# Optimization experiments

Hardware: AMD Instinct MI355X
Metric: run time of the kernel (lower is better)

The kernel has to match this reference:

```python
import jax, jax.numpy as jnp
import numpy as np

NEG_SLOPE = 0.01  # torch nn.LeakyReLU default

N_NODES = 100000
N_EDGES = 1000000
D_FEAT = 64


def setup_inputs() -> dict:
    key = jax.random.key(0)
    ks = jax.random.split(key, 8)
    x = jax.random.normal(ks[0], (N_NODES, D_FEAT), dtype=jnp.float32)
    src = jax.random.randint(ks[1], (N_EDGES,), 0, N_NODES, dtype=jnp.int64 if jax.config.jax_enable_x64 else jnp.int32)
    dst = jax.random.randint(ks[2], (N_EDGES,), 0, N_NODES, dtype=jnp.int64 if jax.config.jax_enable_x64 else jnp.int32)
    s = 1.0 / np.sqrt(D_FEAT)
    W1 = jax.random.normal(ks[3], (D_FEAT, 64), dtype=jnp.float32) * s
    b1 = jnp.zeros((64,), dtype=jnp.float32)
    W2 = jax.random.normal(ks[4], (64, 64), dtype=jnp.float32) * s
    b2 = jnp.zeros((64,), dtype=jnp.float32)
    Wc = jax.random.normal(ks[5], (64, 2), dtype=jnp.float32) * s
    bc = jnp.zeros((2,), dtype=jnp.float32)
    return {"x": x, "src": src, "dst": dst, "W1": W1, "b1": b1,
            "W2": W2, "b2": b2, "Wc": Wc, "bc": bc}


def _graph_conv(x, src, dst, W, b, out_deg_isqrt, in_deg_isqrt, n_nodes):
    # DGL GraphConv, norm='both': h_v = ( sum_{u->v} x_u / sqrt(d_out(u)) ) / sqrt(d_in(v)) @ W + b
    # (in_feats <= out_feats here, so aggregate first then transform, matching DGL order)
    h = x * out_deg_isqrt[:, None]          # [N, d] scale by source out-degree
    msg = h[src]                            # [E, d] gather
    agg = jax.ops.segment_sum(msg, dst, num_segments=n_nodes)  # [N, d] scatter-add
    agg = agg * in_deg_isqrt[:, None]
    return agg @ W + b


def reference(x, src, dst, W1, b1, W2, b2, Wc, bc):
    n = x.shape[0]
    ones_e = jnp.ones(src.shape[0], dtype=x.dtype)
    out_deg = jnp.clip(jax.ops.segment_sum(ones_e, src, num_segments=n), 1.0)
    in_deg = jnp.clip(jax.ops.segment_sum(ones_e, dst, num_segments=n), 1.0)
    out_isqrt = out_deg ** -0.5
    in_isqrt = in_deg ** -0.5

    h = _graph_conv(x, src, dst, W1, b1, out_isqrt, in_isqrt, n)
    h = jax.nn.leaky_relu(h, NEG_SLOPE)
    h = _graph_conv(h, src, dst, W2, b2, out_isqrt, in_isqrt, n)
    h = jax.nn.leaky_relu(h, NEG_SLOPE)
    return h @ Wc + bc  # prediction=True -> linear classifier
```

## Files before the change

### kernel.cpp

```cpp
#include <hip/hip_runtime.h>


typedef __attribute__((ext_vector_type(8))) short short8;
typedef __attribute__((ext_vector_type(4))) float f32x4;

#define NPB 256
#define BSH 9
#define BW  512

__device__ __forceinline__ float b2f(unsigned short u) {
    return __uint_as_float(((unsigned int)u) << 16);
}
__device__ __forceinline__ unsigned short f2b(float f) {
    unsigned int i = __float_as_uint(f);
    unsigned int r = (i + 0x7FFFu + ((i >> 16) & 1u)) >> 16;
    return (unsigned short)r;
}

__global__ __launch_bounds__(256) void count_kernel(
    const int* __restrict__ src, const int* __restrict__ dst,
    int* __restrict__ cntD, int* __restrict__ cntS, int e, int chunk) {
    __shared__ int hD[256], hS[256];
    int t = threadIdx.x, pb = blockIdx.x;
    hD[t] = 0; hS[t] = 0;
    __syncthreads();
    int e0 = pb * chunk, e1 = min(e, e0 + chunk);
    for (int i = e0 + t; i < e1; i += 256) {
        atomicAdd(&hD[dst[i] >> BSH], 1);
        atomicAdd(&hS[src[i] >> BSH], 1);
    }
    __syncthreads();
    cntD[t * NPB + pb] = hD[t];
    cntS[t * NPB + pb] = hS[t];
}

__global__ __launch_bounds__(1024) void scanmat_kernel(int* __restrict__ cntD,
                                                       int* __restrict__ cntS) {
    int* a = (blockIdx.x == 0) ? cntD : cntS;
    __shared__ int s[1024];
    int t = threadIdx.x;
    int base = t * 64;
    int sum = 0;
    for (int j = 0; j < 64; j++) sum += a[base + j];
    s[t] = sum;
    __syncthreads();
    for (int d = 1; d < 1024; d <<= 1) {
        int x = (t >= d) ? s[t - d] : 0;
        __syncthreads();
        s[t] += x;
        __syncthreads();
    }
    int run = s[t] - sum;
    for (int j = 0; j < 64; j++) {
        int v = a[base + j];
        a[base + j] = run;
        run += v;
    }
}

__global__ __launch_bounds__(256) void part_kernel(
    const int* __restrict__ src, const int* __restrict__ dst,
    const int* __restrict__ cntD, const int* __restrict__ cntS,
    unsigned int* __restrict__ ebuf, unsigned short* __restrict__ sbuf,
    int e, int chunk) {
    __shared__ int cD[256], cS[256];
    int t = threadIdx.x, pb = blockIdx.x;
    cD[t] = cntD[t * NPB + pb];
    cS[t] = cntS[t * NPB + pb];
    __syncthreads();
    int e0 = pb * chunk, e1 = min(e, e0 + chunk);
    for (int i = e0 + t; i < e1; i += 256) {
        int s_ = src[i], d_ = dst[i];
        int pd = atomicAdd(&cD[d_ >> BSH], 1);
        ebuf[pd] = ((unsigned int)s_ << BSH) | (unsigned int)(d_ & (BW - 1));
        int ps_ = atomicAdd(&cS[s_ >> BSH], 1);
        sbuf[ps_] = (unsigned short)(s_ & (BW - 1));
    }
}

__global__ __launch_bounds__(256) void bucket_kernel(
    const unsigned int* __restrict__ ebuf, const unsigned short* __restrict__ sbuf,
    const int* __restrict__ cntD, const int* __restrict__ cntS,
    const float4* __restrict__ x4,
    int* __restrict__ row, float* __restrict__ ii, float* __restrict__ oi,
    int* __restrict__ csr, ushort4* __restrict__ xb, int n, int e) {
    __shared__ int cnt[BW], cur[BW], ocnt[BW], ps[256];
    __shared__ float ol[BW];
    int t = threadIdx.x, b = blockIdx.x;
    int v0 = b << BSH;
    int eb0 = cntD[b * NPB], eb1 = cntD[(b + 1) * NPB];
    int sb0 = cntS[b * NPB], sb1 = cntS[(b + 1) * NPB];
    cnt[t] = 0; cnt[t + 256] = 0;
    ocnt[t] = 0; ocnt[t + 256] = 0;
    __syncthreads();
    for (int i = eb0 + t; i < eb1; i += 256)
        atomicAdd(&cnt[ebuf[i] & (BW - 1)], 1);
    for (int i = sb0 + t; i < sb1; i += 256)
        atomicAdd(&ocnt[sbuf[i]], 1);
    __syncthreads();
    int c0 = cnt[2 * t], c1 = cnt[2 * t + 1];
    int pair = c0 + c1;
    ps[t] = pair;
    __syncthreads();
    for (int d = 1; d < 256; d <<= 1) {
        int x = (t >= d) ? ps[t - d] : 0;
        __syncthreads();
        ps[t] += x;
        __syncthreads();
    }
    int excl = ps[t] - pair;
    cur[2 * t] = excl;
    cur[2 * t + 1] = excl + c0;
    int v = v0 + 2 * t;
    if (v < n) {
        row[v] = eb0 + excl;
        ii[v] = rsqrtf((float)max(c0, 1));
    }
    if (v + 1 < n) {
        row[v + 1] = eb0 + excl + c0;
        ii[v + 1] = rsqrtf((float)max(c1, 1));
    }
    if (b == 0 && t == 0) row[n] = e;
    for (int j = t; j < BW; j += 256) {
        float o = rsqrtf((float)max(ocnt[j], 1));
        ol[j] = o;
        int vv = v0 + j;
        if (vv < n) oi[vv] = o;
    }
    __syncthreads();
    for (int i = eb0 + t; i < eb1; i += 256) {
        unsigned int p = ebuf[i];
        int r = atomicAdd(&cur[p & (BW - 1)], 1);
        csr[eb0 + r] = (int)(p >> BSH);
    }
    int nloc = min(BW, n - v0);
    for (int i = t; i < nloc * 16; i += 256) {
        int vl = i >> 4, q = i & 15;
        float s = ol[vl];
        float4 val = x4[(size_t)(v0 + vl) * 16 + q];
        xb[(size_t)(v0 + vl) * 16 + q] =
            make_ushort4(f2b(val.x * s), f2b(val.y * s), f2b(val.z * s), f2b(val.w * s));
    }
}

template <bool FINAL>
__global__ __launch_bounds__(256) void fused_kernel(
    const short8* __restrict__ featb, const int* __restrict__ row,
    const int* __restrict__ csr, const float* __restrict__ ii,
    const float* __restrict__ oi,
    const float* __restrict__ W, const float* __restrict__ bias,
    const float* __restrict__ Wc, const float* __restrict__ bcl,
    void* __restrict__ out, int n, int nwaves) {
    __shared__ short8 tile[4][16 * 9];
    int lane = threadIdx.x & 63;
    int o = lane >> 3, s = lane & 7;
    int m15 = lane & 15, quad = lane >> 4;
    short8* tl = tile[threadIdx.x >> 6];
    int wid = blockIdx.x * (blockDim.x >> 6) + (threadIdx.x >> 6);
    int ngroups = (n + 15) >> 4;

    short8 bf[4][2];
#pragma unroll
    for (int nt = 0; nt < 4; nt++)
#pragma unroll
        for (int kk = 0; kk < 2; kk++)
#pragma unroll
            for (int j = 0; j < 8; j++)
                bf[nt][kk][j] = (short)f2b(W[(kk * 32 + quad * 8 + j) * 64 + nt * 16 + m15]);

    float bias_r[4];
#pragma unroll
    for (int nt = 0; nt < 4; nt++) bias_r[nt] = bias[nt * 16 + m15];

    float wc_r[4][2];
    float bc0 = 0.f, bc1 = 0.f;
    if constexpr (FINAL) {
#pragma unroll
        for (int nt = 0; nt < 4; nt++) {
            wc_r[nt][0] = Wc[(nt * 16 + m15) * 2];
            wc_r[nt][1] = Wc[(nt * 16 + m15) * 2 + 1];
        }
        bc0 = bcl[0];
        bc1 = bcl[1];
    }

    for (int g = wid; g < ngroups; g += nwaves) {
        int rbase = g << 4;

#pragma unroll
        for (int p = 0; p < 2; p++) {
            int v = rbase + p * 8 + o;
            bool valid = v < n;
            int base = 0, cnt = 0;
            if (valid) { base = row[v]; cnt = row[v + 1] - base; }
            float a[8];
#pragma unroll
            for (int k = 0; k < 8; k++) a[k] = 0.f;
            int j = 0;
            for (; j + 3 < cnt; j += 4) {
                int u[4];
#pragma unroll
                for (int k = 0; k < 4; k++) u[k] = csr[base + j + k];
#pragma unroll
                for (int k = 0; k < 4; k++) {
                    short8 f = featb[(size_t)u[k] * 8 + s];
#pragma unroll
                    for (int m = 0; m < 8; m++)
                        a[m] += b2f((unsigned short)f[m]);
                }
            }
            for (; j < cnt; j++) {
                short8 f = featb[(size_t)csr[base + j] * 8 + s];
#pragma unroll
                for (int m = 0; m < 8; m++)
                    a[m] += b2f((unsigned short)f[m]);
            }
            float iiv = valid ? ii[v] : 0.f;
            short8 r;
#pragma unroll
            for (int m = 0; m < 8; m++) r[m] = (short)f2b(a[m] * iiv);
            tl[(p * 8 + o) * 9 + s] = r;
        }

        short8 af0 = tl[m15 * 9 + quad];
        short8 af1 = tl[m15 * 9 + 4 + quad];

        f32x4 acc[4];
#pragma unroll
        for (int nt = 0; nt < 4; nt++) {
            f32x4 z = {0.f, 0.f, 0.f, 0.f};
            z = __builtin_amdgcn_mfma_f32_16x16x32_bf16(af0, bf[nt][0], z, 0, 0, 0);
            z = __builtin_amdgcn_mfma_f32_16x16x32_bf16(af1, bf[nt][1], z, 0, 0, 0);
            acc[nt] = z;
        }

        if constexpr (!FINAL) {
#pragma unroll
            for (int r = 0; r < 4; r++) {
                int vr = rbase + quad * 4 + r;
                float os = (vr < n) ? oi[vr] : 0.f;
#pragma unroll
                for (int nt = 0; nt < 4; nt++) {
                    float ov = acc[nt][r] + bias_r[nt];
                    ov = (ov > 0.f) ? ov : 0.01f * ov;
                    if (vr < n)
                        ((unsigned short*)out)[(size_t)vr * 64 + nt * 16 + m15] = f2b(ov * os);
                }
            }
        } else {
#pragma unroll
            for (int r = 0; r < 4; r++) {
                float p0 = 0.f, p1 = 0.f;
#pragma unroll
                for (int nt = 0; nt < 4; nt++) {
                    float ov = acc[nt][r] + bias_r[nt];
                    ov = (ov > 0.f) ? ov : 0.01f * ov;
                    p0 = fmaf(ov, wc_r[nt][0], p0);
                    p1 = fmaf(ov, wc_r[nt][1], p1);
                }
#pragma unroll
                for (int off = 1; off < 16; off <<= 1) {
                    p0 += __shfl_xor(p0, off);
                    p1 += __shfl_xor(p1, off);
                }
                int vr = rbase + quad * 4 + r;
                if (m15 == 0 && vr < n)
                    ((float2*)out)[vr] = make_float2(p0 + bc0, p1 + bc1);
            }
        }
    }
}

extern "C" void kernel_launch(void* const* d_in, const int* in_sizes, int n_in,
                              void* d_out, int out_size, void* d_ws, size_t ws_size,
                              hipStream_t stream) {
    const float* x  = (const float*)d_in[0];
    const int* src  = (const int*)d_in[1];
    const int* dst  = (const int*)d_in[2];
    const float* W1 = (const float*)d_in[3];
    const float* b1 = (const float*)d_in[4];
    const float* W2 = (const float*)d_in[5];
    const float* b2 = (const float*)d_in[6];
    const float* Wc = (const float*)d_in[7];
    const float* bc = (const float*)d_in[8];
    int n = in_sizes[0] / 64;
    int e = in_sizes[1];
    int total = n * 64;
    int nbuck = (n + BW - 1) >> BSH;

    char* ws = (char*)d_ws;
    size_t off = 0;
    auto take = [&](size_t bytes) -> char* {
        char* p = ws + off;
        off = (off + bytes + 255) & ~(size_t)255;
        return p;
    };
    int* cntD = (int*)take(256 * NPB * 4);
    int* cntS = (int*)take(256 * NPB * 4);
    unsigned int* ebuf = (unsigned int*)take((size_t)e * 4);
    unsigned short* sbuf = (unsigned short*)take((size_t)e * 2);
    int* row  = (int*)take((size_t)(n + 1) * 4);
    int* csr  = (int*)take((size_t)e * 4);
    float* oi = (float*)take((size_t)n * 4);
    float* ii = (float*)take((size_t)n * 4);
    unsigned short* xb  = (unsigned short*)take((size_t)total * 2);
    unsigned short* h1b = (unsigned short*)take((size_t)total * 2);

    const int tb = 256;
    int chunk = (e + NPB - 1) / NPB;

    count_kernel<<<NPB, tb, 0, stream>>>(src, dst, cntD, cntS, e, chunk);
    scanmat_kernel<<<2, 1024, 0, stream>>>(cntD, cntS);
    part_kernel<<<NPB, tb, 0, stream>>>(src, dst, cntD, cntS, ebuf, sbuf, e, chunk);
    bucket_kernel<<<nbuck, tb, 0, stream>>>(ebuf, sbuf, cntD, cntS, (const float4*)x,
                                            row, ii, oi, csr, (ushort4*)xb, n, e);

    const int fblocks = 784;
    const int fwaves = fblocks * (tb / 64);

    fused_kernel<false><<<fblocks, tb, 0, stream>>>((const short8*)xb, row, csr, ii, oi,
                                                    W1, b1, nullptr, nullptr, h1b, n, fwaves);
    fused_kernel<true><<<fblocks, tb, 0, stream>>>((const short8*)h1b, row, csr, ii, nullptr,
                                                   W2, b2, Wc, bc, d_out, n, fwaves);
}
```

Baseline: 221.8 us.

## Vectorize edge preprocessing, split x conversion into own kernel, double fused grid

The count and partition kernels now use 1024-thread blocks and read src/dst as int4 vectors, and the chunk size is rounded to a multiple of four to keep those loads aligned. The matrix scan keeps its segment in registers and uses vectorized loads and stores. The bf16 conversion of x moves out of the bucket kernel into a separate grid-stride kernel, which removes the long per-bucket tail loop at the cost of one extra launch. The fused layer kernels are launched with twice as many blocks. Several unrelated tuning ideas are combined, so gains in one stage may be offset by changed atomic contention or the added launch.

```diff
diff --git a/kernel.cpp b/kernel.cpp
--- a/kernel.cpp
+++ b/kernel.cpp
@@ -5,6 +5,7 @@
 typedef __attribute__((ext_vector_type(4))) float f32x4;
 
 #define NPB 256
+#define SEG 64
 #define BSH 9
 #define BW  512
 
@@ -17,31 +18,51 @@
     return (unsigned short)r;
 }
 
-__global__ __launch_bounds__(256) void count_kernel(
+__global__ __launch_bounds__(1024) void count_kernel(
     const int* __restrict__ src, const int* __restrict__ dst,
     int* __restrict__ cntD, int* __restrict__ cntS, int e, int chunk) {
     __shared__ int hD[256], hS[256];
     int t = threadIdx.x, pb = blockIdx.x;
-    hD[t] = 0; hS[t] = 0;
+    if (t < 256) { hD[t] = 0; hS[t] = 0; }
     __syncthreads();
     int e0 = pb * chunk, e1 = min(e, e0 + chunk);
-    for (int i = e0 + t; i < e1; i += 256) {
+    for (int i = e0 + 4 * t; i + 3 < e1; i += 4096) {
+        int4 d4 = *(const int4*)(dst + i);
+        int4 s4 = *(const int4*)(src + i);
+        atomicAdd(&hD[d4.x >> BSH], 1);
+        atomicAdd(&hD[d4.y >> BSH], 1);
+        atomicAdd(&hD[d4.z >> BSH], 1);
+        atomicAdd(&hD[d4.w >> BSH], 1);
+        atomicAdd(&hS[s4.x >> BSH], 1);
+        atomicAdd(&hS[s4.y >> BSH], 1);
+        atomicAdd(&hS[s4.z >> BSH], 1);
+        atomicAdd(&hS[s4.w >> BSH], 1);
+    }
+    int tb0 = e0 + ((e1 - e0) & ~3);
+    for (int i = tb0 + t; i < e1; i += 1024) {
         atomicAdd(&hD[dst[i] >> BSH], 1);
         atomicAdd(&hS[src[i] >> BSH], 1);
     }
     __syncthreads();
-    cntD[t * NPB + pb] = hD[t];
-    cntS[t * NPB + pb] = hS[t];
+    if (t < 256) {
+        cntD[t * NPB + pb] = hD[t];
+        cntS[t * NPB + pb] = hS[t];
+    }
 }
 
 __global__ __launch_bounds__(1024) void scanmat_kernel(int* __restrict__ cntD,
                                                        int* __restrict__ cntS) {
     int* a = (blockIdx.x == 0) ? cntD : cntS;
+    int4* a4 = (int4*)a;
     __shared__ int s[1024];
     int t = threadIdx.x;
-    int base = t * 64;
+    int4 v[SEG / 4];
     int sum = 0;
-    for (int j = 0; j < 64; j++) sum += a[base + j];
+#pragma unroll
+    for (int j = 0; j < SEG / 4; j++) {
+        v[j] = a4[t * (SEG / 4) + j];
+        sum += v[j].x + v[j].y + v[j].z + v[j].w;
+    }
     s[t] = sum;
     __syncthreads();
     for (int d = 1; d < 1024; d <<= 1) {
@@ -51,25 +72,45 @@
         __syncthreads();
     }
     int run = s[t] - sum;
-    for (int j = 0; j < 64; j++) {
-        int v = a[base + j];
-        a[base + j] = run;
-        run += v;
-    }
-}
-
-__global__ __launch_bounds__(256) void part_kernel(
+#pragma unroll
+    for (int j = 0; j < SEG / 4; j++) {
+        int p0 = run;
+        int p1 = p0 + v[j].x;
+        int p2 = p1 + v[j].y;
+        int p3 = p2 + v[j].z;
+        run = p3 + v[j].w;
+        a4[t * (SEG / 4) + j] = make_int4(p0, p1, p2, p3);
+    }
+}
+
+__global__ __launch_bounds__(1024) void part_kernel(
     const int* __restrict__ src, const int* __restrict__ dst,
     const int* __restrict__ cntD, const int* __restrict__ cntS,
     unsigned int* __restrict__ ebuf, unsigned short* __restrict__ sbuf,
     int e, int chunk) {
     __shared__ int cD[256], cS[256];
     int t = threadIdx.x, pb = blockIdx.x;
-    cD[t] = cntD[t * NPB + pb];
-    cS[t] = cntS[t * NPB + pb];
+    if (t < 256) {
+        cD[t] = cntD[t * NPB + pb];
+        cS[t] = cntS[t * NPB + pb];
+    }
     __syncthreads();
     int e0 = pb * chunk, e1 = min(e, e0 + chunk);
-    for (int i = e0 + t; i < e1; i += 256) {
+    for (int i = e0 + 4 * t; i + 3 < e1; i += 4096) {
+        int4 d4 = *(const int4*)(dst + i);
+        int4 s4 = *(const int4*)(src + i);
+#pragma unroll
+        for (int k = 0; k < 4; k++) {
+            int s_ = (k == 0) ? s4.x : (k == 1) ? s4.y : (k == 2) ? s4.z : s4.w;
+            int d_ = (k == 0) ? d4.x : (k == 1) ? d4.y : (k == 2) ? d4.z : d4.w;
+            int pd = atomicAdd(&cD[d_ >> BSH], 1);
+            ebuf[pd] = ((unsigned int)s_ << BSH) | (unsigned int)(d_ & (BW - 1));
+            int ps_ = atomicAdd(&cS[s_ >> BSH], 1);
+            sbuf[ps_] = (unsigned short)(s_ & (BW - 1));
+        }
+    }
+    int tb0 = e0 + ((e1 - e0) & ~3);
+    for (int i = tb0 + t; i < e1; i += 1024) {
         int s_ = src[i], d_ = dst[i];
         int pd = atomicAdd(&cD[d_ >> BSH], 1);
         ebuf[pd] = ((unsigned int)s_ << BSH) | (unsigned int)(d_ & (BW - 1));
@@ -81,11 +122,9 @@
 __global__ __launch_bounds__(256) void bucket_kernel(
     const unsigned int* __restrict__ ebuf, const unsigned short* __restrict__ sbuf,
     const int* __restrict__ cntD, const int* __restrict__ cntS,
-    const float4* __restrict__ x4,
     int* __restrict__ row, float* __restrict__ ii, float* __restrict__ oi,
-    int* __restrict__ csr, ushort4* __restrict__ xb, int n, int e) {
+    int* __restrict__ csr, int n, int e) {
     __shared__ int cnt[BW], cur[BW], ocnt[BW], ps[256];
-    __shared__ float ol[BW];
     int t = threadIdx.x, b = blockIdx.x;
     int v0 = b << BSH;
     int eb0 = cntD[b * NPB], eb1 = cntD[(b + 1) * NPB];
@@ -122,10 +161,8 @@
     }
     if (b == 0 && t == 0) row[n] = e;
     for (int j = t; j < BW; j += 256) {
-        float o = rsqrtf((float)max(ocnt[j], 1));
-        ol[j] = o;
         int vv = v0 + j;
-        if (vv < n) oi[vv] = o;
+        if (vv < n) oi[vv] = rsqrtf((float)max(ocnt[j], 1));
     }
     __syncthreads();
     for (int i = eb0 + t; i < eb1; i += 256) {
@@ -133,13 +170,17 @@
         int r = atomicAdd(&cur[p & (BW - 1)], 1);
         csr[eb0 + r] = (int)(p >> BSH);
     }
-    int nloc = min(BW, n - v0);
-    for (int i = t; i < nloc * 16; i += 256) {
-        int vl = i >> 4, q = i & 15;
-        float s = ol[vl];
-        float4 val = x4[(size_t)(v0 + vl) * 16 + q];
-        xb[(size_t)(v0 + vl) * 16 + q] =
-            make_ushort4(f2b(val.x * s), f2b(val.y * s), f2b(val.z * s), f2b(val.w * s));
+}
+
+__global__ __launch_bounds__(256) void xconv_kernel(
+    const float4* __restrict__ x4, const float* __restrict__ oi,
+    ushort4* __restrict__ xb, int total4) {
+    int stride = gridDim.x * blockDim.x;
+    for (int i = blockIdx.x * blockDim.x + threadIdx.x; i < total4; i += stride) {
+        float s = oi[i >> 4];
+        float4 val = x4[i];
+        xb[i] = make_ushort4(f2b(val.x * s), f2b(val.y * s),
+                             f2b(val.z * s), f2b(val.w * s));
     }
 }
 
@@ -306,20 +347,21 @@
     unsigned short* xb  = (unsigned short*)take((size_t)total * 2);
     unsigned short* h1b = (unsigned short*)take((size_t)total * 2);
 
-    const int tb = 256;
-    int chunk = (e + NPB - 1) / NPB;
-
-    count_kernel<<<NPB, tb, 0, stream>>>(src, dst, cntD, cntS, e, chunk);
+    int chunk = (((e + NPB - 1) / NPB) + 3) & ~3;
+
+    count_kernel<<<NPB, 1024, 0, stream>>>(src, dst, cntD, cntS, e, chunk);
     scanmat_kernel<<<2, 1024, 0, stream>>>(cntD, cntS);
-    part_kernel<<<NPB, tb, 0, stream>>>(src, dst, cntD, cntS, ebuf, sbuf, e, chunk);
-    bucket_kernel<<<nbuck, tb, 0, stream>>>(ebuf, sbuf, cntD, cntS, (const float4*)x,
-                                            row, ii, oi, csr, (ushort4*)xb, n, e);
-
-    const int fblocks = 784;
-    const int fwaves = fblocks * (tb / 64);
-
-    fused_kernel<false><<<fblocks, tb, 0, stream>>>((const short8*)xb, row, csr, ii, oi,
-                                                    W1, b1, nullptr, nullptr, h1b, n, fwaves);
-    fused_kernel<true><<<fblocks, tb, 0, stream>>>((const short8*)h1b, row, csr, ii, nullptr,
-                                                   W2, b2, Wc, bc, d_out, n, fwaves);
-}
+    part_kernel<<<NPB, 1024, 0, stream>>>(src, dst, cntD, cntS, ebuf, sbuf, e, chunk);
+    bucket_kernel<<<nbuck, 256, 0, stream>>>(ebuf, sbuf, cntD, cntS,
+                                             row, ii, oi, csr, n, e);
+    xconv_kernel<<<2048, 256, 0, stream>>>((const float4*)x, oi, (ushort4*)xb,
+                                           n * 16);
+
+    const int fblocks = 1568;
+    const int fwaves = fblocks * (256 / 64);
+
+    fused_kernel<false><<<fblocks, 256, 0, stream>>>((const short8*)xb, row, csr, ii, oi,
+                                                     W1, b1, nullptr, nullptr, h1b, n, fwaves);
+    fused_kernel<true><<<fblocks, 256, 0, stream>>>((const short8*)h1b, row, csr, ii, nullptr,
+                                                    W2, b2, Wc, bc, d_out, n, fwaves);
+}
```

After: 207.4 us. 6.5% less time.
